# Kernel tuning notes

Hardware: AMD Instinct MI355X
Metric: run time of the kernel (lower is better)

## Reference

```python
import jax, jax.numpy as jnp
import numpy as np

B, S, D, H, CS = 2, 4096, 1024, 16, 128
HD = D // H            # head_dim = 64
C = S // CS            # num_chunks = 32
NEG = -1e9


def setup_inputs() -> dict:
    key = jax.random.key(0)
    ks = jax.random.split(key, 13)
    w = lambda k: jax.random.normal(k, (D, D), jnp.float32) * 0.02
    b = lambda k: jax.random.normal(k, (D,), jnp.float32) * 0.02
    return {
        'hidden_states': jax.random.normal(ks[0], (B, S, D), jnp.float32),
        'Wq': w(ks[1]), 'bq': b(ks[2]),
        'Wk': w(ks[3]), 'bk': b(ks[4]),
        'Wv': w(ks[5]), 'bv': b(ks[6]),
        'Wo': w(ks[7]), 'bo': b(ks[8]),
        'Wr': w(ks[9]), 'br': b(ks[10]),
        'Wh': w(ks[11]), 'bh': b(ks[12]),
    }


def reference(hidden_states, Wq, bq, Wk, bk, Wv, bv, Wo, bo, Wr, br, Wh, bh):
    scale = 1.0 / np.sqrt(HD)
    proj = lambda x, W, bias: x @ W.T + bias  # torch nn.Linear convention

    # QKV, split heads: [B,H,C,CS,HD]
    def heads(x):
        return x.reshape(B, S, H, HD).transpose(0, 2, 1, 3).reshape(B, H, C, CS, HD)
    qc = heads(proj(hidden_states, Wq, bq))
    kc = heads(proj(hidden_states, Wk, bk))
    vc = heads(proj(hidden_states, Wv, bv))

    # Chunk representation = last token of each chunk (no padding since S % CS == 0)
    chunk_repr = hidden_states.reshape(B, C, CS, D)[:, :, -1, :]  # [B,C,D]
    r = proj(chunk_repr, Wr, br).reshape(B, C, H, HD).transpose(0, 2, 1, 3)  # [B,H,C,HD]
    h = proj(chunk_repr, Wh, bh).reshape(B, C, H, HD).transpose(0, 2, 1, 3)

    # Compressed chunk states F = K^T V per chunk: [B,H,C,HD,HD]
    f = jnp.einsum('bhcsd,bhcse->bhcde', kc, vc)

    # Inter-chunk retrieval (module uses triu mask: chunk i attends chunks j >= i)
    chunk_scores = jnp.einsum('bhcd,bhed->bhce', r, h) * scale  # [B,H,C,C]
    m_out = jnp.triu(jnp.ones((C, C), jnp.float32))
    chunk_scores = jnp.where(m_out == 0, NEG, chunk_scores)
    chunk_probs = jax.nn.softmax(chunk_scores, axis=-1)
    retrieved = jnp.einsum('bhce,bhexy->bhcxy', chunk_probs, f)  # [B,H,C,HD,HD]
    long_term = jnp.einsum('bhcsd,bhcde->bhcse', qc, retrieved)  # [B,H,C,CS,HD]

    # Intra-chunk attention, block-diagonal (mask is triu within chunk)
    local_scores = jnp.einsum('bhcsd,bhctd->bhcst', qc, kc) * scale  # [B,H,C,CS,CS]
    m_in = jnp.triu(jnp.ones((CS, CS), jnp.float32))
    local_scores = jnp.where(m_in == 0, NEG, local_scores)
    local_probs = jax.nn.softmax(local_scores, axis=-1)
    local_out = jnp.einsum('bhcst,bhctd->bhcsd', local_probs, vc)

    out = (long_term + local_out).reshape(B, H, S, HD).transpose(0, 2, 1, 3).reshape(B, S, D)
    return out @ Wo.T + bo
```

## Files before the change

### kernel.cpp

```cpp
#include <hip/hip_runtime.h>
#include <stdint.h>

#define NEG9 (-1e9f)

typedef __attribute__((ext_vector_type(8))) short short8;
typedef __attribute__((ext_vector_type(8))) unsigned short ushort8;
typedef __attribute__((ext_vector_type(4))) unsigned short ushort4_t;
typedef __attribute__((ext_vector_type(4))) float f32x4;

#define MFMA_BF16(a,b,c) __builtin_amdgcn_mfma_f32_16x16x32_bf16((a),(b),(c),0,0,0)

__device__ __forceinline__ unsigned short f2bf(float f) {
  union { float f; unsigned int u; } x; x.f = f;
  unsigned int r = x.u + 0x7fffu + ((x.u >> 16) & 1u);
  return (unsigned short)(r >> 16);
}
__device__ __forceinline__ float bf2f(unsigned short h) {
  union { unsigned int u; float f; } x; x.u = ((unsigned int)h) << 16;
  return x.f;
}
__device__ __forceinline__ void gload_lds16(const unsigned short* g, unsigned short* l) {
  __builtin_amdgcn_global_load_lds(
      (const __attribute__((address_space(1))) unsigned int*)g,
      (__attribute__((address_space(3))) unsigned int*)l, 16, 0, 0);
}

__global__ void cvt_f32_bf16(const float* __restrict__ in, unsigned short* __restrict__ out, int n4) {
  int i = blockIdx.x * blockDim.x + threadIdx.x;
  int stride = gridDim.x * blockDim.x;
  for (; i < n4; i += stride) {
    float4 v = ((const float4*)in)[i];
    ushort4_t o;
    o.x = f2bf(v.x); o.y = f2bf(v.y); o.z = f2bf(v.z); o.w = f2bf(v.w);
    ((ushort4_t*)out)[i] = o;
  }
}

__global__ void cvt_w6(const float* a0, const float* a1, const float* a2,
                       const float* a3, const float* a4, const float* a5,
                       unsigned short* b0, unsigned short* b1, unsigned short* b2,
                       unsigned short* b3, unsigned short* b4, unsigned short* b5) {
  const float* in; unsigned short* out;
  switch (blockIdx.y) {
    case 0: in = a0; out = b0; break;
    case 1: in = a1; out = b1; break;
    case 2: in = a2; out = b2; break;
    case 3: in = a3; out = b3; break;
    case 4: in = a4; out = b4; break;
    default: in = a5; out = b5; break;
  }
  const int n4 = 262144;
  int i = blockIdx.x * blockDim.x + threadIdx.x;
  int stride = gridDim.x * blockDim.x;
  for (; i < n4; i += stride) {
    float4 v = ((const float4*)in)[i];
    ushort4_t o;
    o.x = f2bf(v.x); o.y = f2bf(v.y); o.z = f2bf(v.z); o.w = f2bf(v.w);
    ((ushort4_t*)out)[i] = o;
  }
}

template<int OUT_F32>
__global__ __launch_bounds__(256)
void gemm_bt(const unsigned short* __restrict__ A,
             const unsigned short* __restrict__ W,
             const float* __restrict__ bias,
             void* __restrict__ Cout,
             int M, int N, int K) {
  __shared__ unsigned short As[128*32];
  __shared__ unsigned short Bs[128*32];
  const int t = threadIdx.x;
  const int lane = t & 63;
  const int wave = t >> 6;
  const int wr = wave >> 1, wc = wave & 1;
  const int lr = lane & 15;
  const int lk = (lane >> 4) << 3;

  const int nbn = N >> 7;
  const int nwg = (M >> 7) * nbn;
  int bid = blockIdx.x;
  if ((nwg & 7) == 0) { int q = nwg >> 3; bid = (bid & 7) * q + (bid >> 3); }
  const int bm = bid / nbn, bn = bid % nbn;

  const long rowA0 = (long)bm * 128;
  const long rowB0 = (long)bn * 128;
  const int srow = t >> 2;
  const int scol = (t & 3) << 3;

  f32x4 acc[4][4];
#pragma unroll
  for (int m = 0; m < 4; m++)
#pragma unroll
    for (int n = 0; n < 4; n++) acc[m][n] = f32x4{0.f,0.f,0.f,0.f};

  for (int k0 = 0; k0 < K; k0 += 32) {
    const unsigned short* ga = A + (rowA0 + srow) * K + k0 + scol;
    const unsigned short* gb = W + (rowB0 + srow) * K + k0 + scol;
    gload_lds16(ga,              As + t*8);
    gload_lds16(ga + (long)64*K, As + t*8 + 2048);
    gload_lds16(gb,              Bs + t*8);
    gload_lds16(gb + (long)64*K, Bs + t*8 + 2048);
    __syncthreads();
    short8 af[4], bf[4];
#pragma unroll
    for (int m = 0; m < 4; m++) af[m] = *(const short8*)&As[(wr*64 + m*16 + lr)*32 + lk];
#pragma unroll
    for (int n = 0; n < 4; n++) bf[n] = *(const short8*)&Bs[(wc*64 + n*16 + lr)*32 + lk];
#pragma unroll
    for (int m = 0; m < 4; m++)
#pragma unroll
      for (int n = 0; n < 4; n++)
        acc[m][n] = MFMA_BF16(af[m], bf[n], acc[m][n]);
    __syncthreads();
  }

  const int rg4 = (lane >> 4) * 4;
#pragma unroll
  for (int m = 0; m < 4; m++) {
#pragma unroll
    for (int n = 0; n < 4; n++) {
      long row = rowA0 + wr*64 + m*16 + rg4;
      long col = rowB0 + wc*64 + n*16 + lr;
      float bv = bias[col];
#pragma unroll
      for (int r = 0; r < 4; r++) {
        float v = acc[m][n][r] + bv;
        if (OUT_F32) ((float*)Cout)[(row + r) * N + col] = v;
        else ((unsigned short*)Cout)[(row + r) * N + col] = f2bf(v);
      }
    }
  }
}

__global__ void repr_pad(const float* __restrict__ hs, unsigned short* __restrict__ out) {
  int r = blockIdx.x;
  int t = threadIdx.x;
  long base = (long)r * 1024;
  if (r < 64) {
    int b = r >> 5, c = r & 31;
    const float* src = hs + ((long)(b*4096 + c*128 + 127)) * 1024;
#pragma unroll
    for (int j = 0; j < 4; j++) { int idx = t + j*256; out[base + idx] = f2bf(src[idx]); }
  } else {
#pragma unroll
    for (int j = 0; j < 4; j++) out[base + t + j*256] = 0;
  }
}

__global__ __launch_bounds__(1024) void chunk_probs_k(
    const unsigned short* __restrict__ rb,
    const unsigned short* __restrict__ hb,
    float* __restrict__ probs) {
  __shared__ float rt[32][65];
  __shared__ float ht[32][65];
  int h = blockIdx.x, b = blockIdx.y;
  int t = threadIdx.x;
#pragma unroll
  for (int j = 0; j < 2; j++) {
    int idx = t + j*1024;
    int c = idx >> 6, d = idx & 63;
    rt[c][d] = bf2f(rb[(long)(b*32 + c)*1024 + h*64 + d]);
    ht[c][d] = bf2f(hb[(long)(b*32 + c)*1024 + h*64 + d]);
  }
  __syncthreads();
  int e = t & 31, c = t >> 5;
  float s = 0.f;
#pragma unroll
  for (int d = 0; d < 64; d++) s += rt[c][d] * ht[e][d];
  s *= 0.125f;
  if (e < c) s = NEG9;
  float m = s;
#pragma unroll
  for (int off = 16; off > 0; off >>= 1) m = fmaxf(m, __shfl_xor(m, off, 32));
  float p = __expf(s - m);
  float sum = p;
#pragma unroll
  for (int off = 16; off > 0; off >>= 1) sum += __shfl_xor(sum, off, 32);
  probs[(((long)(b*16 + h))*32 + c)*32 + e] = p / sum;
}

__global__ __launch_bounds__(256) void f_kernel(
    const unsigned short* __restrict__ Kb, const unsigned short* __restrict__ Vb,
    unsigned short* __restrict__ f) {
  __shared__ unsigned short vT[64*136];
  __shared__ unsigned short kT[64*136];
  int bid = blockIdx.x;
  int c = bid & 31, h = (bid >> 5) & 15, b = bid >> 9;
  int t = threadIdx.x;
  const unsigned short* kg = Kb + ((long)(b*4096 + c*128))*1024 + h*64;
  const unsigned short* vg = Vb + ((long)(b*4096 + c*128))*1024 + h*64;
  {
    int s = t >> 1, e0 = (t & 1) << 5;
#pragma unroll
    for (int j = 0; j < 4; j++) {
      ushort8 v = *(const ushort8*)&vg[(long)s*1024 + e0 + j*8];
      ushort8 k = *(const ushort8*)&kg[(long)s*1024 + e0 + j*8];
#pragma unroll
      for (int x = 0; x < 8; x++) {
        vT[(e0 + j*8 + x)*136 + s] = v[x];
        kT[(e0 + j*8 + x)*136 + s] = k[x];
      }
    }
  }
  __syncthreads();
  const int lane = t & 63, w = t >> 6;
  const int lr = lane & 15, lk = (lane >> 4) << 3;
  const int rg4 = (lane >> 4) * 4;
  const int e0w = (w & 1) * 32, d0w = (w >> 1) * 32;

  f32x4 acc[2][2];
#pragma unroll
  for (int m = 0; m < 2; m++)
#pragma unroll
    for (int n = 0; n < 2; n++) acc[m][n] = f32x4{0.f,0.f,0.f,0.f};
#pragma unroll
  for (int kk = 0; kk < 4; kk++) {
    short8 af[2], bf[2];
#pragma unroll
    for (int m = 0; m < 2; m++) af[m] = *(const short8*)&vT[(e0w + m*16 + lr)*136 + kk*32 + lk];
#pragma unroll
    for (int n = 0; n < 2; n++) bf[n] = *(const short8*)&kT[(d0w + n*16 + lr)*136 + kk*32 + lk];
#pragma unroll
    for (int m = 0; m < 2; m++)
#pragma unroll
      for (int n = 0; n < 2; n++) acc[m][n] = MFMA_BF16(af[m], bf[n], acc[m][n]);
  }
  unsigned short* fo = f + (long)bid * 4096;
#pragma unroll
  for (int m = 0; m < 2; m++)
#pragma unroll
    for (int n = 0; n < 2; n++)
#pragma unroll
      for (int r = 0; r < 4; r++)
        fo[(e0w + m*16 + rg4 + r)*64 + d0w + n*16 + lr] = f2bf(acc[m][n][r]);
}

__global__ __launch_bounds__(256) void retrieve_k(
    const float* __restrict__ probs, const unsigned short* __restrict__ f,
    unsigned short* __restrict__ retT) {
  __shared__ float PL[1024];
  int bh = blockIdx.x;
  int xt = blockIdx.y;
  int t = threadIdx.x;
  *(float4*)&PL[t*4] = *(const float4*)&probs[(long)bh*1024 + t*4];
  __syncthreads();
  const unsigned int* fb = (const unsigned int*)(f + (long)bh*32*4096);
  const int xo = xt*256 + t;
  unsigned int fv[32];
#pragma unroll
  for (int ec = 0; ec < 32; ec++) fv[ec] = fb[ec*2048 + xo];
  unsigned int* ro = (unsigned int*)retT + (long)bh*32*2048 + xo;
  for (int c = 0; c < 32; c++) {
    float a0 = 0.f, a1 = 0.f;
#pragma unroll
    for (int e4 = 0; e4 < 8; e4++) {
      float4 p = *(const float4*)&PL[c*32 + e4*4];
#pragma unroll
      for (int j = 0; j < 4; j++) {
        unsigned int v = fv[e4*4 + j];
        union { unsigned int u; float ff; } lo, hi;
        lo.u = v << 16; hi.u = v & 0xffff0000u;
        a0 += p[j] * lo.ff;
        a1 += p[j] * hi.ff;
      }
    }
    ro[(long)c*2048] = (unsigned int)f2bf(a0) | ((unsigned int)f2bf(a1) << 16);
  }
}

__global__ __launch_bounds__(256) void attn_k(
    const unsigned short* __restrict__ Qb,
    const unsigned short* __restrict__ Kb,
    const unsigned short* __restrict__ Vb,
    const unsigned short* __restrict__ retT,
    unsigned short* __restrict__ attn) {
  __shared__ unsigned short ks[128*64];
  __shared__ unsigned short vT[64*136];
  __shared__ unsigned short rT[64*64];
  __shared__ unsigned short P[128*136];
  const int bid = blockIdx.x;
  const int c = bid & 31, h = (bid >> 5) & 15, b = bid >> 9;
  const int t = threadIdx.x;
  const int lane = t & 63, w = t >> 6;
  const int lr = lane & 15, lk = (lane >> 4) << 3;
  const int rg4 = (lane >> 4) * 4;

  const long rowbase = (long)(b*4096 + c*128);
  const unsigned short* kg = Kb + rowbase*1024 + h*64;
  const unsigned short* vg = Vb + rowbase*1024 + h*64;
  const unsigned short* qg = Qb + rowbase*1024 + h*64;
  const unsigned short* rtg = retT + (long)bid*4096;

  {
    int sr = t >> 3, scc = (t & 7) << 3;
#pragma unroll
    for (int i = 0; i < 4; i++)
      gload_lds16(kg + (long)(sr + i*32)*1024 + scc, ks + t*8 + i*2048);
#pragma unroll
    for (int i = 0; i < 2; i++)
      gload_lds16(rtg + (t + i*256)*8, rT + (t + i*256)*8);
  }
  {
    int s = t >> 1, e0 = (t & 1) << 5;
#pragma unroll
    for (int jj = 0; jj < 4; jj++) {
      ushort8 v = *(const ushort8*)&vg[(long)s*1024 + e0 + jj*8];
#pragma unroll
      for (int x = 0; x < 8; x++) vT[(e0 + jj*8 + x)*136 + s] = v[x];
    }
  }
  __syncthreads();

  short8 qa[2][2];
#pragma unroll
  for (int m = 0; m < 2; m++)
#pragma unroll
    for (int kk = 0; kk < 2; kk++)
      qa[m][kk] = *(const short8*)&qg[(long)(w*32 + m*16 + lr)*1024 + kk*32 + lk];
  f32x4 scf[2][8];
#pragma unroll
  for (int m = 0; m < 2; m++)
#pragma unroll
    for (int n = 0; n < 8; n++) scf[m][n] = f32x4{0.f,0.f,0.f,0.f};
#pragma unroll
  for (int n = 0; n < 8; n++) {
#pragma unroll
    for (int kk = 0; kk < 2; kk++) {
      short8 kf = *(const short8*)&ks[(n*16 + lr)*64 + kk*32 + lk];
#pragma unroll
      for (int m = 0; m < 2; m++) scf[m][n] = MFMA_BF16(qa[m][kk], kf, scf[m][n]);
    }
  }

  float rsum[2][4];
#pragma unroll
  for (int m = 0; m < 2; m++) {
#pragma unroll
    for (int r = 0; r < 4; r++) {
      int srow = w*32 + m*16 + rg4 + r;
      float vals[8];
      float mx = -1e30f;
#pragma unroll
      for (int n = 0; n < 8; n++) {
        int tcol = n*16 + lr;
        float v_ = scf[m][n][r] * 0.125f;
        if (tcol < srow) v_ = NEG9;
        vals[n] = v_;
        mx = fmaxf(mx, v_);
      }
#pragma unroll
      for (int off = 1; off < 16; off <<= 1) mx = fmaxf(mx, __shfl_xor(mx, off, 16));
      float sum = 0.f;
#pragma unroll
      for (int n = 0; n < 8; n++) {
        float p = __expf(vals[n] - mx);
        sum += p;
        P[srow*136 + n*16 + lr] = f2bf(p);
      }
#pragma unroll
      for (int off = 1; off < 16; off <<= 1) sum += __shfl_xor(sum, off, 16);
      rsum[m][r] = sum;
    }
  }

  f32x4 outa[2][4];
#pragma unroll
  for (int m = 0; m < 2; m++)
#pragma unroll
    for (int n = 0; n < 4; n++) outa[m][n] = f32x4{0.f,0.f,0.f,0.f};
#pragma unroll
  for (int n = 0; n < 4; n++) {
#pragma unroll
    for (int kk = 0; kk < 2; kk++) {
      short8 rf = *(const short8*)&rT[(n*16 + lr)*64 + kk*32 + lk];
#pragma unroll
      for (int m = 0; m < 2; m++) outa[m][n] = MFMA_BF16(qa[m][kk], rf, outa[m][n]);
    }
  }

  f32x4 pv[2][4];
#pragma unroll
  for (int m = 0; m < 2; m++)
#pragma unroll
    for (int n = 0; n < 4; n++) pv[m][n] = f32x4{0.f,0.f,0.f,0.f};
#pragma unroll
  for (int kk = 0; kk < 4; kk++) {
    short8 pa[2];
#pragma unroll
    for (int m = 0; m < 2; m++) pa[m] = *(const short8*)&P[(w*32 + m*16 + lr)*136 + kk*32 + lk];
#pragma unroll
    for (int n = 0; n < 4; n++) {
      short8 vf = *(const short8*)&vT[(n*16 + lr)*136 + kk*32 + lk];
#pragma unroll
      for (int m = 0; m < 2; m++) pv[m][n] = MFMA_BF16(pa[m], vf, pv[m][n]);
    }
  }

  unsigned short* ao = attn + rowbase*1024 + h*64;
#pragma unroll
  for (int m = 0; m < 2; m++)
#pragma unroll
    for (int n = 0; n < 4; n++)
#pragma unroll
      for (int r = 0; r < 4; r++) {
        int srow = w*32 + m*16 + rg4 + r;
        float v_ = pv[m][n][r] / rsum[m][r] + outa[m][n][r];
        ao[(long)srow*1024 + n*16 + lr] = f2bf(v_);
      }
}

extern "C" void kernel_launch(void* const* d_in, const int* in_sizes, int n_in,
                              void* d_out, int out_size, void* d_ws, size_t ws_size,
                              hipStream_t stream) {
  const float* hs = (const float*)d_in[0];
  const float* Wq = (const float*)d_in[1];
  const float* bq = (const float*)d_in[2];
  const float* Wk = (const float*)d_in[3];
  const float* bk = (const float*)d_in[4];
  const float* Wv = (const float*)d_in[5];
  const float* bv = (const float*)d_in[6];
  const float* Wo = (const float*)d_in[7];
  const float* bo = (const float*)d_in[8];
  const float* Wr = (const float*)d_in[9];
  const float* br = (const float*)d_in[10];
  const float* Wh = (const float*)d_in[11];
  const float* bh = (const float*)d_in[12];

  char* p = (char*)d_ws;
  unsigned short* hsb  = (unsigned short*)p; p += (size_t)8192*1024*2;
  unsigned short* Wqb  = (unsigned short*)p; p += (size_t)1024*1024*2;
  unsigned short* Wkb  = (unsigned short*)p; p += (size_t)1024*1024*2;
  unsigned short* Wvb  = (unsigned short*)p; p += (size_t)1024*1024*2;
  unsigned short* Wob  = (unsigned short*)p; p += (size_t)1024*1024*2;
  unsigned short* Wrb  = (unsigned short*)p; p += (size_t)1024*1024*2;
  unsigned short* Whb  = (unsigned short*)p; p += (size_t)1024*1024*2;
  unsigned short* Qb   = (unsigned short*)p; p += (size_t)8192*1024*2;
  unsigned short* Kb   = (unsigned short*)p; p += (size_t)8192*1024*2;
  unsigned short* Vb   = (unsigned short*)p; p += (size_t)8192*1024*2;
  unsigned short* reprb= (unsigned short*)p; p += (size_t)128*1024*2;
  unsigned short* rb   = (unsigned short*)p; p += (size_t)128*1024*2;
  unsigned short* hb   = (unsigned short*)p; p += (size_t)128*1024*2;
  float*          probs= (float*)p;          p += (size_t)2*16*32*32*4;
  unsigned short* fbuf = (unsigned short*)p; p += (size_t)2*16*32*4096*2;
  unsigned short* retT = (unsigned short*)p; p += (size_t)2*16*32*4096*2;
  unsigned short* attnb = hsb;

  cvt_f32_bf16<<<8192, 256, 0, stream>>>(hs, hsb, 2097152);
  cvt_w6<<<dim3(256, 6), 256, 0, stream>>>(Wq, Wk, Wv, Wo, Wr, Wh,
                                           Wqb, Wkb, Wvb, Wob, Wrb, Whb);

  gemm_bt<0><<<512, 256, 0, stream>>>(hsb, Wqb, bq, Qb, 8192, 1024, 1024);
  gemm_bt<0><<<512, 256, 0, stream>>>(hsb, Wkb, bk, Kb, 8192, 1024, 1024);
  gemm_bt<0><<<512, 256, 0, stream>>>(hsb, Wvb, bv, Vb, 8192, 1024, 1024);

  repr_pad<<<128, 256, 0, stream>>>(hs, reprb);
  gemm_bt<0><<<8, 256, 0, stream>>>(reprb, Wrb, br, rb, 128, 1024, 1024);
  gemm_bt<0><<<8, 256, 0, stream>>>(reprb, Whb, bh, hb, 128, 1024, 1024);

  chunk_probs_k<<<dim3(16, 2), 1024, 0, stream>>>(rb, hb, probs);

  f_kernel<<<1024, 256, 0, stream>>>(Kb, Vb, fbuf);

  retrieve_k<<<dim3(32, 8), 256, 0, stream>>>(probs, fbuf, retT);

  attn_k<<<1024, 256, 0, stream>>>(Qb, Kb, Vb, retT, attnb);

  gemm_bt<1><<<512, 256, 0, stream>>>(attnb, Wob, bo, d_out, 8192, 1024, 1024);
}
```

Measured before the change: 333.7 us.

## Fuse QKV and R/H projections into single GEMMs, vectorize transposes, swizzle LDS

```diff
diff --git a/kernel.cpp b/kernel.cpp
--- a/kernel.cpp
+++ b/kernel.cpp
@@ -132,7 +132,83 @@
   }
 }
 
-__global__ void repr_pad(const float* __restrict__ hs, unsigned short* __restrict__ out) {
+__global__ __launch_bounds__(256)
+void gemm_qkv(const unsigned short* __restrict__ A,
+              const unsigned short* __restrict__ Wqkv,
+              const float* __restrict__ bq, const float* __restrict__ bk,
+              const float* __restrict__ bv,
+              unsigned short* __restrict__ Q, unsigned short* __restrict__ Kb,
+              unsigned short* __restrict__ V) {
+  const int K = 1024;
+  __shared__ unsigned short As[128*32];
+  __shared__ unsigned short Bs[128*32];
+  const int t = threadIdx.x;
+  const int lane = t & 63;
+  const int wave = t >> 6;
+  const int wr = wave >> 1, wc = wave & 1;
+  const int lr = lane & 15;
+  const int lk = (lane >> 4) << 3;
+
+  const int nbn = 24;
+  int bid = blockIdx.x;
+  { int q = 1536 >> 3; bid = (bid & 7) * q + (bid >> 3); }
+  const int bm = bid / nbn, bn = bid % nbn;
+
+  const long rowA0 = (long)bm * 128;
+  const long rowB0 = (long)bn * 128;
+  const int srow = t >> 2;
+  const int scol = (t & 3) << 3;
+
+  f32x4 acc[4][4];
+#pragma unroll
+  for (int m = 0; m < 4; m++)
+#pragma unroll
+    for (int n = 0; n < 4; n++) acc[m][n] = f32x4{0.f,0.f,0.f,0.f};
+
+  for (int k0 = 0; k0 < K; k0 += 32) {
+    const unsigned short* ga = A + (rowA0 + srow) * K + k0 + scol;
+    const unsigned short* gb = Wqkv + (rowB0 + srow) * K + k0 + scol;
+    gload_lds16(ga,              As + t*8);
+    gload_lds16(ga + (long)64*K, As + t*8 + 2048);
+    gload_lds16(gb,              Bs + t*8);
+    gload_lds16(gb + (long)64*K, Bs + t*8 + 2048);
+    __syncthreads();
+    short8 af[4], bf[4];
+#pragma unroll
+    for (int m = 0; m < 4; m++) af[m] = *(const short8*)&As[(wr*64 + m*16 + lr)*32 + lk];
+#pragma unroll
+    for (int n = 0; n < 4; n++) bf[n] = *(const short8*)&Bs[(wc*64 + n*16 + lr)*32 + lk];
+#pragma unroll
+    for (int m = 0; m < 4; m++)
+#pragma unroll
+      for (int n = 0; n < 4; n++)
+        acc[m][n] = MFMA_BF16(af[m], bf[n], acc[m][n]);
+    __syncthreads();
+  }
+
+  const int which = bn >> 3;
+  unsigned short* Co = (which == 0) ? Q : (which == 1) ? Kb : V;
+  const float* bsel = (which == 0) ? bq : (which == 1) ? bk : bv;
+  const long colbase = rowB0 - (long)which * 1024;
+
+  const int rg4 = (lane >> 4) * 4;
+#pragma unroll
+  for (int m = 0; m < 4; m++) {
+#pragma unroll
+    for (int n = 0; n < 4; n++) {
+      long row = rowA0 + wr*64 + m*16 + rg4;
+      long col = colbase + wc*64 + n*16 + lr;
+      float bvv = bsel[col];
+#pragma unroll
+      for (int r = 0; r < 4; r++)
+        Co[(row + r) * 1024 + col] = f2bf(acc[m][n][r] + bvv);
+    }
+  }
+}
+
+__global__ void repr_pad(const float* __restrict__ hs, unsigned short* __restrict__ out,
+                         const float* __restrict__ br, const float* __restrict__ bh,
+                         float* __restrict__ brh) {
   int r = blockIdx.x;
   int t = threadIdx.x;
   long base = (long)r * 1024;
@@ -144,12 +220,18 @@
   } else {
 #pragma unroll
     for (int j = 0; j < 4; j++) out[base + t + j*256] = 0;
+    if (r == 64) {
+#pragma unroll
+      for (int j = 0; j < 4; j++) { int idx = t + j*256; brh[idx] = br[idx]; }
+    } else if (r == 65) {
+#pragma unroll
+      for (int j = 0; j < 4; j++) { int idx = t + j*256; brh[1024 + idx] = bh[idx]; }
+    }
   }
 }
 
 __global__ __launch_bounds__(1024) void chunk_probs_k(
-    const unsigned short* __restrict__ rb,
-    const unsigned short* __restrict__ hb,
+    const unsigned short* __restrict__ rbh,
     float* __restrict__ probs) {
   __shared__ float rt[32][65];
   __shared__ float ht[32][65];
@@ -159,8 +241,8 @@
   for (int j = 0; j < 2; j++) {
     int idx = t + j*1024;
     int c = idx >> 6, d = idx & 63;
-    rt[c][d] = bf2f(rb[(long)(b*32 + c)*1024 + h*64 + d]);
-    ht[c][d] = bf2f(hb[(long)(b*32 + c)*1024 + h*64 + d]);
+    rt[c][d] = bf2f(rbh[(long)(b*32 + c)*2048 + h*64 + d]);
+    ht[c][d] = bf2f(rbh[(long)(b*32 + c)*2048 + 1024 + h*64 + d]);
   }
   __syncthreads();
   int e = t & 31, c = t >> 5;
@@ -190,16 +272,21 @@
   const unsigned short* kg = Kb + ((long)(b*4096 + c*128))*1024 + h*64;
   const unsigned short* vg = Vb + ((long)(b*4096 + c*128))*1024 + h*64;
   {
-    int s = t >> 1, e0 = (t & 1) << 5;
-#pragma unroll
-    for (int j = 0; j < 4; j++) {
-      ushort8 v = *(const ushort8*)&vg[(long)s*1024 + e0 + j*8];
-      ushort8 k = *(const ushort8*)&kg[(long)s*1024 + e0 + j*8];
-#pragma unroll
-      for (int x = 0; x < 8; x++) {
-        vT[(e0 + j*8 + x)*136 + s] = v[x];
-        kT[(e0 + j*8 + x)*136 + s] = k[x];
-      }
+    int eq = t & 7, sq = t >> 3;
+    int s0 = sq*4, e0 = eq*8;
+    ushort8 v[4], k[4];
+#pragma unroll
+    for (int r = 0; r < 4; r++) {
+      v[r] = *(const ushort8*)&vg[(long)(s0 + r)*1024 + e0];
+      k[r] = *(const ushort8*)&kg[(long)(s0 + r)*1024 + e0];
+    }
+#pragma unroll
+    for (int x = 0; x < 8; x++) {
+      ushort4_t pv, pk;
+      pv.x = v[0][x]; pv.y = v[1][x]; pv.z = v[2][x]; pv.w = v[3][x];
+      pk.x = k[0][x]; pk.y = k[1][x]; pk.z = k[2][x]; pk.w = k[3][x];
+      *(ushort4_t*)&vT[(e0 + x)*136 + s0] = pv;
+      *(ushort4_t*)&kT[(e0 + x)*136 + s0] = pk;
     }
   }
   __syncthreads();
@@ -292,21 +379,31 @@
   const unsigned short* rtg = retT + (long)bid*4096;
 
   {
-    int sr = t >> 3, scc = (t & 7) << 3;
-#pragma unroll
-    for (int i = 0; i < 4; i++)
-      gload_lds16(kg + (long)(sr + i*32)*1024 + scc, ks + t*8 + i*2048);
-#pragma unroll
-    for (int i = 0; i < 2; i++)
-      gload_lds16(rtg + (t + i*256)*8, rT + (t + i*256)*8);
+    const int off = (t & 7) << 4;
+#pragma unroll
+    for (int i = 0; i < 4; i++) {
+      int row = (t >> 3) + i*32;
+      int srcoff = off ^ ((row & 7) << 4);
+      gload_lds16(kg + (long)row*1024 + (srcoff >> 1), ks + t*8 + i*2048);
+    }
+#pragma unroll
+    for (int i = 0; i < 2; i++) {
+      int row = ((t + i*256) >> 3);
+      int srcoff = off ^ ((row & 7) << 4);
+      gload_lds16(rtg + (long)row*64 + (srcoff >> 1), rT + (t + i*256)*8);
+    }
   }
   {
-    int s = t >> 1, e0 = (t & 1) << 5;
-#pragma unroll
-    for (int jj = 0; jj < 4; jj++) {
-      ushort8 v = *(const ushort8*)&vg[(long)s*1024 + e0 + jj*8];
-#pragma unroll
-      for (int x = 0; x < 8; x++) vT[(e0 + jj*8 + x)*136 + s] = v[x];
+    int eq = t & 7, sq = t >> 3;
+    int s0 = sq*4, e0 = eq*8;
+    ushort8 v[4];
+#pragma unroll
+    for (int r = 0; r < 4; r++) v[r] = *(const ushort8*)&vg[(long)(s0 + r)*1024 + e0];
+#pragma unroll
+    for (int x = 0; x < 8; x++) {
+      ushort4_t pv;
+      pv.x = v[0][x]; pv.y = v[1][x]; pv.z = v[2][x]; pv.w = v[3][x];
+      *(ushort4_t*)&vT[(e0 + x)*136 + s0] = pv;
     }
   }
   __syncthreads();
@@ -324,9 +421,12 @@
     for (int n = 0; n < 8; n++) scf[m][n] = f32x4{0.f,0.f,0.f,0.f};
 #pragma unroll
   for (int n = 0; n < 8; n++) {
+    const int krow = n*16 + lr;
+    const int swzmask = (krow & 7) << 4;
 #pragma unroll
     for (int kk = 0; kk < 2; kk++) {
-      short8 kf = *(const short8*)&ks[(n*16 + lr)*64 + kk*32 + lk];
+      int colb = (kk*64 + ((lane >> 4) << 4)) ^ swzmask;
+      short8 kf = *(const short8*)&ks[krow*64 + (colb >> 1)];
 #pragma unroll
       for (int m = 0; m < 2; m++) scf[m][n] = MFMA_BF16(qa[m][kk], kf, scf[m][n]);
     }
@@ -370,9 +470,12 @@
     for (int n = 0; n < 4; n++) outa[m][n] = f32x4{0.f,0.f,0.f,0.f};
 #pragma unroll
   for (int n = 0; n < 4; n++) {
+    const int rrow = n*16 + lr;
+    const int swzmask = (rrow & 7) << 4;
 #pragma unroll
     for (int kk = 0; kk < 2; kk++) {
-      short8 rf = *(const short8*)&rT[(n*16 + lr)*64 + kk*32 + lk];
+      int colb = (kk*64 + ((lane >> 4) << 4)) ^ swzmask;
+      short8 rf = *(const short8*)&rT[rrow*64 + (colb >> 1)];
 #pragma unroll
       for (int m = 0; m < 2; m++) outa[m][n] = MFMA_BF16(qa[m][kk], rf, outa[m][n]);
     }
@@ -428,18 +531,15 @@
 
   char* p = (char*)d_ws;
   unsigned short* hsb  = (unsigned short*)p; p += (size_t)8192*1024*2;
-  unsigned short* Wqb  = (unsigned short*)p; p += (size_t)1024*1024*2;
-  unsigned short* Wkb  = (unsigned short*)p; p += (size_t)1024*1024*2;
-  unsigned short* Wvb  = (unsigned short*)p; p += (size_t)1024*1024*2;
+  unsigned short* Wqkv = (unsigned short*)p; p += (size_t)3072*1024*2;
   unsigned short* Wob  = (unsigned short*)p; p += (size_t)1024*1024*2;
-  unsigned short* Wrb  = (unsigned short*)p; p += (size_t)1024*1024*2;
-  unsigned short* Whb  = (unsigned short*)p; p += (size_t)1024*1024*2;
+  unsigned short* Wrh  = (unsigned short*)p; p += (size_t)2048*1024*2;
   unsigned short* Qb   = (unsigned short*)p; p += (size_t)8192*1024*2;
   unsigned short* Kb   = (unsigned short*)p; p += (size_t)8192*1024*2;
   unsigned short* Vb   = (unsigned short*)p; p += (size_t)8192*1024*2;
   unsigned short* reprb= (unsigned short*)p; p += (size_t)128*1024*2;
-  unsigned short* rb   = (unsigned short*)p; p += (size_t)128*1024*2;
-  unsigned short* hb   = (unsigned short*)p; p += (size_t)128*1024*2;
+  unsigned short* rbhb = (unsigned short*)p; p += (size_t)128*2048*2;
+  float*          brh  = (float*)p;          p += (size_t)2048*4;
   float*          probs= (float*)p;          p += (size_t)2*16*32*32*4;
   unsigned short* fbuf = (unsigned short*)p; p += (size_t)2*16*32*4096*2;
   unsigned short* retT = (unsigned short*)p; p += (size_t)2*16*32*4096*2;
@@ -447,17 +547,16 @@
 
   cvt_f32_bf16<<<8192, 256, 0, stream>>>(hs, hsb, 2097152);
   cvt_w6<<<dim3(256, 6), 256, 0, stream>>>(Wq, Wk, Wv, Wo, Wr, Wh,
-                                           Wqb, Wkb, Wvb, Wob, Wrb, Whb);
-
-  gemm_bt<0><<<512, 256, 0, stream>>>(hsb, Wqb, bq, Qb, 8192, 1024, 1024);
-  gemm_bt<0><<<512, 256, 0, stream>>>(hsb, Wkb, bk, Kb, 8192, 1024, 1024);
-  gemm_bt<0><<<512, 256, 0, stream>>>(hsb, Wvb, bv, Vb, 8192, 1024, 1024);
-
-  repr_pad<<<128, 256, 0, stream>>>(hs, reprb);
-  gemm_bt<0><<<8, 256, 0, stream>>>(reprb, Wrb, br, rb, 128, 1024, 1024);
-  gemm_bt<0><<<8, 256, 0, stream>>>(reprb, Whb, bh, hb, 128, 1024, 1024);
-
-  chunk_probs_k<<<dim3(16, 2), 1024, 0, stream>>>(rb, hb, probs);
+                                           Wqkv, Wqkv + (size_t)1024*1024,
+                                           Wqkv + (size_t)2048*1024,
+                                           Wob, Wrh, Wrh + (size_t)1024*1024);
+  repr_pad<<<128, 256, 0, stream>>>(hs, reprb, br, bh, brh);
+
+  gemm_qkv<<<1536, 256, 0, stream>>>(hsb, Wqkv, bq, bk, bv, Qb, Kb, Vb);
+
+  gemm_bt<0><<<16, 256, 0, stream>>>(reprb, Wrh, brh, rbhb, 128, 2048, 1024);
+
+  chunk_probs_k<<<dim3(16, 2), 1024, 0, stream>>>(rbhb, probs);
 
   f_kernel<<<1024, 256, 0, stream>>>(Kb, Vb, fbuf);
 
```

Result: faster. 293.2 us (-12.1%).
